# Optimization experiments

Measured on AMD Instinct MI355X. Metric: run time of the kernel, lower is better.

The kernel has to match this reference:

```python
import jax, jax.numpy as jnp
import numpy as np

DIM = 512
N_EMBED = 4096
B, T = 16, 4096


def setup_inputs() -> dict:
    key = jax.random.key(0)
    kx, ke = jax.random.split(key)
    x = jax.random.normal(kx, (B, T, DIM), dtype=jnp.float32)
    embed = jax.random.normal(ke, (DIM, N_EMBED), dtype=jnp.float32)  # codebook buffer
    return {"x": x, "embed": embed}


def reference(x, embed):
    dim = x.shape[-1]
    flatten = x.reshape(-1, dim)  # [N, dim]
    # squared L2 distance to each codebook vector: ||f||^2 - 2 f.e + ||e||^2
    dist = (
        jnp.sum(flatten * flatten, axis=1, keepdims=True)
        - 2.0 * (flatten @ embed)
        + jnp.sum(embed * embed, axis=0, keepdims=True)
    )  # [N, n_embed]
    embed_ind = jnp.argmin(dist, axis=1).reshape(x.shape[:-1])  # [B, T]
    quantize = jnp.take(embed.T, embed_ind, axis=0)  # [B, T, dim]
    diff = jnp.mean((jax.lax.stop_gradient(quantize) - x) ** 2)
    # straight-through estimator
    quantize_st = x + jax.lax.stop_gradient(quantize - x)
    return quantize_st, diff, embed_ind
```

## Files before the change

### kernel.cpp

```cpp
#include <hip/hip_runtime.h>
#include <math.h>

#define DIM 512
#define NE 4096
#define NROWS 65536
#define MARGIN 0.6f

typedef __attribute__((ext_vector_type(8))) short short8;
typedef __attribute__((ext_vector_type(4))) float f32x4;

__device__ inline unsigned short f2bf(float f) {
    union { float f; unsigned int u; } v; v.f = f;
    unsigned int u = v.u;
    return (unsigned short)((u + 0x7fffu + ((u >> 16) & 1u)) >> 16);
}
__device__ inline float bf2f(unsigned short h) {
    union { unsigned int u; float f; } v; v.u = ((unsigned int)h) << 16;
    return v.f;
}
__device__ inline short hi_bf(float f) { return (short)f2bf(f); }

__device__ inline bool lexlt(float v1, int i1, float v2, int i2) {
    return (v1 < v2) || (v1 == v2 && i1 < i2);
}

__device__ __forceinline__ size_t ehf_idx(int e, int d) {
    return (size_t)(e >> 5) * 16384 +
           (size_t)(((((d >> 5) * 2 + ((e >> 4) & 1)) * 64) + ((d >> 3) & 3) * 16 + (e & 15)) * 8 + (d & 7));
}

typedef __attribute__((address_space(1))) const void gconst_t;
typedef __attribute__((address_space(3))) void ldsv_t;
__device__ __forceinline__ void gload_lds16(const void* g, void* l) {
    __builtin_amdgcn_global_load_lds((gconst_t*)g, (ldsv_t*)l, 16, 0, 0);
}

__global__ void norms_kernel(const float* __restrict__ embed, float* __restrict__ norms) {
    int e = blockIdx.x * blockDim.x + threadIdx.x;
    if (e < NE) {
        float s = 0.f;
        #pragma unroll 8
        for (int d = 0; d < DIM; ++d) {
            float v = embed[(size_t)d * NE + e];
            s += v * v;
        }
        norms[e] = s;
    }
}

__global__ void prep_kernel(const float* __restrict__ embed,
                            unsigned short* __restrict__ ehf,
                            unsigned short* __restrict__ el) {
    __shared__ float t[64][65];
    const int tid = threadIdx.x;
    const int e0 = blockIdx.x * 64;
    const int d0 = blockIdx.y * 64;
    for (int i = tid; i < 4096; i += 256) {
        int r = i >> 6, c = i & 63;
        t[r][c] = embed[(size_t)(d0 + r) * NE + e0 + c];
    }
    __syncthreads();
    for (int i = tid; i < 4096; i += 256) {
        int r = i >> 6, c = i & 63;
        float v = t[c][r];
        int e = e0 + r, d = d0 + c;
        unsigned short h = f2bf(v);
        ehf[ehf_idx(e, d)] = h;
        el[(size_t)e * 512 + d] = f2bf(v - bf2f(h));
    }
}

__global__ __launch_bounds__(256, 2) void vq_main(
        const float* __restrict__ x,
        const unsigned short* __restrict__ ehf,
        const unsigned short* __restrict__ el,
        const float* __restrict__ norms,
        float* __restrict__ out_idx,
        int* __restrict__ idx_ws) {

    __shared__ unsigned short ph[2][32 * 512];
    __shared__ int   bi4[128][4];
    __shared__ float bgap[128];

    const int tid = threadIdx.x;
    const int w   = tid >> 6;
    const int l   = tid & 63;
    const int lr  = l & 15;
    const int lg  = l >> 4;
    const int row0 = blockIdx.x * 128;

    short8 a[2][16];
    #pragma unroll
    for (int s = 0; s < 2; ++s) {
        const float* xp = x + (size_t)(row0 + w * 32 + s * 16 + lr) * DIM + lg * 8;
        #pragma unroll
        for (int ks = 0; ks < 16; ++ks) {
            float4 u  = *(const float4*)(xp + ks * 32);
            float4 v2 = *(const float4*)(xp + ks * 32 + 4);
            short8 h;
            h[0]=hi_bf(u.x);  h[1]=hi_bf(u.y);  h[2]=hi_bf(u.z);  h[3]=hi_bf(u.w);
            h[4]=hi_bf(v2.x); h[5]=hi_bf(v2.y); h[6]=hi_bf(v2.z); h[7]=hi_bf(v2.w);
            a[s][ks] = h;
        }
    }

    float t1v[2][4], t2v[2][4]; int t1i[2][4], t2i[2][4];
    #pragma unroll
    for (int s = 0; s < 2; ++s)
        #pragma unroll
        for (int r = 0; r < 4; ++r) {
            t1v[s][r]=INFINITY; t2v[s][r]=INFINITY;
            t1i[s][r]=0x7ffffffe; t2i[s][r]=0x7fffffff;
        }

    #define STAGE_PANEL(p, b)                                                   \
    {                                                                           \
        const unsigned short* gsrc = ehf + (size_t)(p) * 16384 + w * 4096 + l * 8; \
        unsigned short* ldst = &ph[b][w * 4096];                                \
        _Pragma("unroll")                                                       \
        for (int j = 0; j < 8; ++j)                                             \
            gload_lds16(gsrc + j * 512, ldst + j * 512);                        \
    }

    STAGE_PANEL(0, 0)
    __syncthreads();

    #pragma unroll 1
    for (int ct = 0; ct < 128; ++ct) {
        const int cur = ct & 1;

        if (ct < 127) STAGE_PANEL(ct + 1, cur ^ 1)

        f32x4 acc[2][2];
        #pragma unroll
        for (int s = 0; s < 2; ++s)
            #pragma unroll
            for (int cb = 0; cb < 2; ++cb) acc[s][cb] = (f32x4){0.f,0.f,0.f,0.f};

        #pragma unroll
        for (int ks = 0; ks < 16; ++ks) {
            #pragma unroll
            for (int cb = 0; cb < 2; ++cb) {
                short8 bh = *(const short8*)&ph[cur][(ks * 2 + cb) * 512 + l * 8];
                acc[0][cb] = __builtin_amdgcn_mfma_f32_16x16x32_bf16(a[0][ks], bh, acc[0][cb], 0, 0, 0);
                acc[1][cb] = __builtin_amdgcn_mfma_f32_16x16x32_bf16(a[1][ks], bh, acc[1][cb], 0, 0, 0);
            }
        }

        #pragma unroll
        for (int cb = 0; cb < 2; ++cb) {
            int e = ct * 32 + cb * 16 + lr;
            float nrm = norms[e];
            #pragma unroll
            for (int s = 0; s < 2; ++s)
                #pragma unroll
                for (int r = 0; r < 4; ++r) {
                    float sv = fmaf(-2.0f, acc[s][cb][r], nrm);
                    if (sv < t1v[s][r]) { t2v[s][r]=t1v[s][r]; t2i[s][r]=t1i[s][r]; t1v[s][r]=sv; t1i[s][r]=e; }
                    else if (sv < t2v[s][r]) { t2v[s][r]=sv; t2i[s][r]=e; }
                }
        }
        __syncthreads();
    }
    #undef STAGE_PANEL

    #pragma unroll
    for (int s = 0; s < 2; ++s) {
        #pragma unroll
        for (int r = 0; r < 4; ++r) {
            float av[4] = { t1v[s][r], t2v[s][r], INFINITY, INFINITY };
            int   ai[4] = { t1i[s][r], t2i[s][r], 0x7ffffffe, 0x7fffffff };
            #pragma unroll
            for (int m = 1; m < 16; m <<= 1) {
                float bv[4]; int bi_[4];
                #pragma unroll
                for (int q = 0; q < 4; ++q) {
                    bv[q]  = __shfl_xor(av[q], m, 64);
                    bi_[q] = __shfl_xor(ai[q], m, 64);
                }
                float cv[4]; int ci[4];
                #pragma unroll
                for (int q = 0; q < 4; ++q) {
                    bool t = lexlt(av[q], ai[q], bv[3 - q], bi_[3 - q]);
                    cv[q] = t ? av[q] : bv[3 - q];
                    ci[q] = t ? ai[q] : bi_[3 - q];
                }
                #define CE(A,B) { if (!lexlt(cv[A],ci[A],cv[B],ci[B])) { \
                    float tv=cv[A]; cv[A]=cv[B]; cv[B]=tv; int ti=ci[A]; ci[A]=ci[B]; ci[B]=ti; } }
                CE(0,2) CE(1,3) CE(0,1) CE(2,3)
                #undef CE
                #pragma unroll
                for (int q = 0; q < 4; ++q) { av[q] = cv[q]; ai[q] = ci[q]; }
            }
            if (lr == 0) {
                int rowloc = w * 32 + s * 16 + lg * 4 + r;
                #pragma unroll
                for (int q = 0; q < 4; ++q) bi4[rowloc][q] = ai[q];
                bgap[rowloc] = av[1] - av[0];
            }
        }
    }
    __syncthreads();

    #pragma unroll 1
    for (int rr = 0; rr < 32; ++rr) {
        int rowloc = w * 32 + rr;
        int grow = row0 + rowloc;
        float gap = bgap[rowloc];
        int c0 = bi4[rowloc][0] & (NE - 1);
        if (gap > MARGIN) {
            if (l == 0) { out_idx[grow] = (float)c0; idx_ws[grow] = c0; }
            continue;
        }
        int cand[4];
        cand[0] = c0;
        cand[1] = bi4[rowloc][1] & (NE - 1);
        cand[2] = bi4[rowloc][2] & (NE - 1);
        cand[3] = bi4[rowloc][3] & (NE - 1);

        const float* xr = x + (size_t)grow * DIM + l * 8;
        float4 xa = *(const float4*)xr, xb = *(const float4*)(xr + 4);
        float xv[8] = {xa.x, xa.y, xa.z, xa.w, xb.x, xb.y, xb.z, xb.w};

        float d[4];
        #pragma unroll
        for (int q = 0; q < 4; ++q) {
            uint4 hv = *(const uint4*)&ehf[ehf_idx(cand[q], l * 8)];
            uint4 lv = *(const uint4*)&el[(size_t)cand[q] * 512 + l * 8];
            const unsigned short* hp = (const unsigned short*)&hv;
            const unsigned short* lp = (const unsigned short*)&lv;
            float acc = 0.f;
            #pragma unroll
            for (int j = 0; j < 8; ++j) acc += xv[j] * (bf2f(hp[j]) + bf2f(lp[j]));
            d[q] = acc;
        }
        #pragma unroll
        for (int m = 32; m >= 1; m >>= 1) {
            #pragma unroll
            for (int q = 0; q < 4; ++q) d[q] += __shfl_xor(d[q], m, 64);
        }
        if (l == 0) {
            float bs = norms[cand[0]] - 2.0f * d[0];
            int   bi = cand[0];
            #pragma unroll
            for (int q = 1; q < 4; ++q) {
                float sq = norms[cand[q]] - 2.0f * d[q];
                if (sq < bs || (sq == bs && cand[q] < bi)) { bs = sq; bi = cand[q]; }
            }
            out_idx[grow] = (float)bi;
            idx_ws[grow] = bi;
        }
    }
}

__global__ void gather_kernel(const float* __restrict__ x,
                              const unsigned short* __restrict__ ehf,
                              const unsigned short* __restrict__ el,
                              const int* __restrict__ idx, float* __restrict__ out_q,
                              float* __restrict__ partial) {
    __shared__ float red[256];
    const int tid = threadIdx.x;
    float local = 0.f;
    #pragma unroll 1
    for (int j = 0; j < 8; ++j) {
        int o8 = blockIdx.x * 2048 + j * 256 + tid;
        int r  = o8 >> 6;
        int c8 = o8 & 63;
        int e  = idx[r];
        uint4 hv = *(const uint4*)&ehf[ehf_idx(e, c8 * 8)];
        uint4 lv = *(const uint4*)&el[(size_t)e * 512 + c8 * 8];
        const unsigned short* hp = (const unsigned short*)&hv;
        const unsigned short* lp = (const unsigned short*)&lv;
        float q[8];
        #pragma unroll
        for (int k = 0; k < 8; ++k) q[k] = bf2f(hp[k]) + bf2f(lp[k]);
        float4 xa = *(const float4*)&x[(size_t)r * DIM + c8 * 8];
        float4 xb = *(const float4*)&x[(size_t)r * DIM + c8 * 8 + 4];
        *(float4*)&out_q[(size_t)r * DIM + c8 * 8]     = make_float4(q[0], q[1], q[2], q[3]);
        *(float4*)&out_q[(size_t)r * DIM + c8 * 8 + 4] = make_float4(q[4], q[5], q[6], q[7]);
        float xs[8] = {xa.x, xa.y, xa.z, xa.w, xb.x, xb.y, xb.z, xb.w};
        #pragma unroll
        for (int k = 0; k < 8; ++k) { float t = q[k] - xs[k]; local += t * t; }
    }
    red[tid] = local;
    __syncthreads();
    for (int s = 128; s > 0; s >>= 1) {
        if (tid < s) red[tid] += red[tid + s];
        __syncthreads();
    }
    if (tid == 0) partial[blockIdx.x] = red[0];
}

__global__ void diff_kernel(const float* __restrict__ partial, float* __restrict__ out_diff) {
    __shared__ float red[256];
    float s = 0.f;
    for (int i = threadIdx.x; i < 2048; i += 256) s += partial[i];
    red[threadIdx.x] = s;
    __syncthreads();
    for (int st = 128; st > 0; st >>= 1) {
        if (threadIdx.x < st) red[threadIdx.x] += red[threadIdx.x + st];
        __syncthreads();
    }
    if (threadIdx.x == 0)
        out_diff[0] = red[0] * (1.0f / ((float)NROWS * (float)DIM));
}

#define BM 32
#define BN 64
#define BK 16
__global__ __launch_bounds__(256) void vq_kernel_fb(
        const float* __restrict__ x, const float* __restrict__ embed,
        const float* __restrict__ norms, float* __restrict__ out_q,
        float* __restrict__ out_idx, float* __restrict__ partial) {
    __shared__ float xs[BM][BK + 1];
    __shared__ float es[BK][BN];
    __shared__ float rv[BM][17];
    __shared__ int   ri[BM][17];
    __shared__ float bestv[BM];
    __shared__ int   besti[BM];
    __shared__ float red[256];
    const int tid = threadIdx.x;
    const int tc  = tid & 15;
    const int tr  = tid >> 4;
    const int row0 = blockIdx.x * BM;
    if (tid < BM) { bestv[tid] = INFINITY; besti[tid] = 0; }
    __syncthreads();
    for (int ct = 0; ct < NE / BN; ++ct) {
        float acc[2][4] = {{0.f,0.f,0.f,0.f},{0.f,0.f,0.f,0.f}};
        for (int k0 = 0; k0 < DIM; k0 += BK) {
            {
                int r = tid >> 3;
                int k = (tid & 7) * 2;
                const float* src = &x[(size_t)(row0 + r) * DIM + k0 + k];
                xs[r][k] = src[0]; xs[r][k + 1] = src[1];
            }
            {
                int r = tid >> 4;
                int c = (tid & 15) * 4;
                float4 v = *(const float4*)&embed[(size_t)(k0 + r) * NE + ct * BN + c];
                *(float4*)&es[r][c] = v;
            }
            __syncthreads();
            #pragma unroll
            for (int kk = 0; kk < BK; ++kk) {
                float a0 = xs[tr * 2 + 0][kk];
                float a1 = xs[tr * 2 + 1][kk];
                float4 b = *(const float4*)&es[kk][tc * 4];
                acc[0][0] += a0 * b.x; acc[0][1] += a0 * b.y;
                acc[0][2] += a0 * b.z; acc[0][3] += a0 * b.w;
                acc[1][0] += a1 * b.x; acc[1][1] += a1 * b.y;
                acc[1][2] += a1 * b.z; acc[1][3] += a1 * b.w;
            }
            __syncthreads();
        }
        #pragma unroll
        for (int i = 0; i < 2; ++i) {
            float bv = INFINITY; int bj = 0;
            #pragma unroll
            for (int j = 0; j < 4; ++j) {
                int e = ct * BN + tc * 4 + j;
                float s = norms[e] - 2.0f * acc[i][j];
                if (s < bv) { bv = s; bj = e; }
            }
            rv[tr * 2 + i][tc] = bv; ri[tr * 2 + i][tc] = bj;
        }
        __syncthreads();
        if (tid < BM) {
            float bv = bestv[tid]; int bi = besti[tid];
            #pragma unroll
            for (int t = 0; t < 16; ++t) {
                float v = rv[tid][t];
                if (v < bv) { bv = v; bi = ri[tid][t]; }
            }
            bestv[tid] = bv; besti[tid] = bi;
        }
        __syncthreads();
    }
    if (tid < BM) out_idx[row0 + tid] = (float)besti[tid];
    __syncthreads();
    float local = 0.f;
    for (int i = tid; i < BM * DIM; i += 256) {
        int r = i >> 9;
        int d = i & (DIM - 1);
        int e = besti[r];
        float q  = embed[(size_t)d * NE + e];
        float xv = x[(size_t)(row0 + r) * DIM + d];
        out_q[(size_t)(row0 + r) * DIM + d] = q;
        float t = q - xv;
        local += t * t;
    }
    red[tid] = local;
    __syncthreads();
    for (int s = 128; s > 0; s >>= 1) {
        if (tid < s) red[tid] += red[tid + s];
        __syncthreads();
    }
    if (tid == 0) partial[blockIdx.x] = red[0];
}

extern "C" void kernel_launch(void* const* d_in, const int* in_sizes, int n_in,
                              void* d_out, int out_size, void* d_ws, size_t ws_size,
                              hipStream_t stream) {
    (void)in_sizes; (void)n_in; (void)out_size;
    const float* x     = (const float*)d_in[0];
    const float* embed = (const float*)d_in[1];

    float* out      = (float*)d_out;
    float* out_q    = out;
    float* out_diff = out + (size_t)NROWS * DIM;
    float* out_idx  = out_diff + 1;

    const size_t NEED = 4194304ull * 2 + 16384 + 8192 + 262144;

    char* wsb = (char*)d_ws;
    if (ws_size >= NEED) {
        unsigned short* ehf     = (unsigned short*)wsb;
        unsigned short* el      = (unsigned short*)(wsb + 4194304);
        float*          norms   = (float*)(wsb + 8388608);
        float*          partial = (float*)(wsb + 8404992);
        int*            idx     = (int*)(wsb + 8413184);

        norms_kernel<<<NE / 256, 256, 0, stream>>>(embed, norms);
        prep_kernel<<<dim3(64, 8), 256, 0, stream>>>(embed, ehf, el);
        vq_main<<<512, 256, 0, stream>>>(x, ehf, el, norms, out_idx, idx);
        gather_kernel<<<2048, 256, 0, stream>>>(x, ehf, el, idx, out_q, partial);
        diff_kernel<<<1, 256, 0, stream>>>(partial, out_diff);
    } else {
        float* norms   = (float*)wsb;
        float* partial = norms + NE;
        norms_kernel<<<NE / 256, 256, 0, stream>>>(embed, norms);
        vq_kernel_fb<<<NROWS / BM, 256, 0, stream>>>(x, embed, norms, out_q, out_idx, partial);
        diff_kernel<<<1, 256, 0, stream>>>(partial, out_diff);
    }
}
```

Before: 469.9 us.

## Software-pipeline MFMA with epilogue and pack distance and index into one key

The codebook panel loop now keeps two sets of accumulators. The MFMAs for panel i+1 are issued while the top-2 epilogue for panel i runs, so matrix math overlaps the scalar compare work. The top-2 tracking and the cross-lane merge replace branchy float/index comparisons with branchless unsigned min/max on a single key: the float distance bits with the low 12 mantissa bits replaced by the codebook index. That key truncation costs distance precision, so the rescoring margin is raised from 0.6 to 1.0, which may send more rows to the exact fallback. Ordering raw float bits as unsigned integers is only correct for non-negative distances.

Result: faster. 416.2 us (-11.4%).

```diff
diff --git a/kernel.cpp b/kernel.cpp
--- a/kernel.cpp
+++ b/kernel.cpp
@@ -4,7 +4,7 @@
 #define DIM 512
 #define NE 4096
 #define NROWS 65536
-#define MARGIN 0.6f
+#define MARGIN 1.0f
 
 typedef __attribute__((ext_vector_type(8))) short short8;
 typedef __attribute__((ext_vector_type(4))) float f32x4;
@@ -19,10 +19,6 @@
     return v.f;
 }
 __device__ inline short hi_bf(float f) { return (short)f2bf(f); }
-
-__device__ inline bool lexlt(float v1, int i1, float v2, int i2) {
-    return (v1 < v2) || (v1 == v2 && i1 < i2);
-}
 
 __device__ __forceinline__ size_t ehf_idx(int e, int d) {
     return (size_t)(e >> 5) * 16384 +
@@ -104,99 +100,111 @@
         }
     }
 
-    float t1v[2][4], t2v[2][4]; int t1i[2][4], t2i[2][4];
+    unsigned p1[2][4], p2[2][4];
     #pragma unroll
     for (int s = 0; s < 2; ++s)
         #pragma unroll
-        for (int r = 0; r < 4; ++r) {
-            t1v[s][r]=INFINITY; t2v[s][r]=INFINITY;
-            t1i[s][r]=0x7ffffffe; t2i[s][r]=0x7fffffff;
-        }
-
-    #define STAGE_PANEL(p, b)                                                   \
-    {                                                                           \
+        for (int r = 0; r < 4; ++r) { p1[s][r] = 0xFFFFFFFFu; p2[s][r] = 0xFFFFFFFFu; }
+
+    f32x4 accA[2][2], accB[2][2];
+
+    #define STAGE_PANEL(p, b)                                                      \
+    {                                                                              \
         const unsigned short* gsrc = ehf + (size_t)(p) * 16384 + w * 4096 + l * 8; \
-        unsigned short* ldst = &ph[b][w * 4096];                                \
-        _Pragma("unroll")                                                       \
-        for (int j = 0; j < 8; ++j)                                             \
-            gload_lds16(gsrc + j * 512, ldst + j * 512);                        \
+        unsigned short* ldst = &ph[b][w * 4096];                                   \
+        _Pragma("unroll")                                                          \
+        for (int j = 0; j < 8; ++j)                                                \
+            gload_lds16(gsrc + j * 512, ldst + j * 512);                           \
+    }
+
+    #define MFMA_PANEL(ACC, BUF)                                                   \
+    {                                                                              \
+        _Pragma("unroll")                                                          \
+        for (int s = 0; s < 2; ++s)                                                \
+            _Pragma("unroll")                                                      \
+            for (int cb = 0; cb < 2; ++cb) ACC[s][cb] = (f32x4){0.f,0.f,0.f,0.f};  \
+        _Pragma("unroll")                                                          \
+        for (int ks = 0; ks < 16; ++ks) {                                          \
+            _Pragma("unroll")                                                      \
+            for (int cb = 0; cb < 2; ++cb) {                                       \
+                short8 bh = *(const short8*)&ph[BUF][(ks * 2 + cb) * 512 + l * 8]; \
+                ACC[0][cb] = __builtin_amdgcn_mfma_f32_16x16x32_bf16(a[0][ks], bh, ACC[0][cb], 0, 0, 0); \
+                ACC[1][cb] = __builtin_amdgcn_mfma_f32_16x16x32_bf16(a[1][ks], bh, ACC[1][cb], 0, 0, 0); \
+            }                                                                      \
+        }                                                                          \
+    }
+
+    #define EPIL_PANEL(ACC, PANEL)                                                 \
+    {                                                                              \
+        _Pragma("unroll")                                                          \
+        for (int cb = 0; cb < 2; ++cb) {                                           \
+            int e = (PANEL) * 32 + cb * 16 + lr;                                   \
+            float nrm = norms[e];                                                  \
+            _Pragma("unroll")                                                      \
+            for (int s = 0; s < 2; ++s)                                            \
+                _Pragma("unroll")                                                  \
+                for (int r = 0; r < 4; ++r) {                                      \
+                    float sv = fmaf(-2.0f, ACC[s][cb][r], nrm);                    \
+                    unsigned pv = (__float_as_uint(sv) & 0xFFFFF000u) | (unsigned)e; \
+                    unsigned t = max(p1[s][r], pv);                                \
+                    p1[s][r] = min(p1[s][r], pv);                                  \
+                    p2[s][r] = min(p2[s][r], t);                                   \
+                }                                                                  \
+        }                                                                          \
     }
 
     STAGE_PANEL(0, 0)
     __syncthreads();
+    STAGE_PANEL(1, 1)
+    MFMA_PANEL(accA, 0)
+    __syncthreads();
 
     #pragma unroll 1
-    for (int ct = 0; ct < 128; ++ct) {
-        const int cur = ct & 1;
-
-        if (ct < 127) STAGE_PANEL(ct + 1, cur ^ 1)
-
-        f32x4 acc[2][2];
-        #pragma unroll
-        for (int s = 0; s < 2; ++s)
-            #pragma unroll
-            for (int cb = 0; cb < 2; ++cb) acc[s][cb] = (f32x4){0.f,0.f,0.f,0.f};
-
-        #pragma unroll
-        for (int ks = 0; ks < 16; ++ks) {
-            #pragma unroll
-            for (int cb = 0; cb < 2; ++cb) {
-                short8 bh = *(const short8*)&ph[cur][(ks * 2 + cb) * 512 + l * 8];
-                acc[0][cb] = __builtin_amdgcn_mfma_f32_16x16x32_bf16(a[0][ks], bh, acc[0][cb], 0, 0, 0);
-                acc[1][cb] = __builtin_amdgcn_mfma_f32_16x16x32_bf16(a[1][ks], bh, acc[1][cb], 0, 0, 0);
-            }
-        }
-
-        #pragma unroll
-        for (int cb = 0; cb < 2; ++cb) {
-            int e = ct * 32 + cb * 16 + lr;
-            float nrm = norms[e];
-            #pragma unroll
-            for (int s = 0; s < 2; ++s)
-                #pragma unroll
-                for (int r = 0; r < 4; ++r) {
-                    float sv = fmaf(-2.0f, acc[s][cb][r], nrm);
-                    if (sv < t1v[s][r]) { t2v[s][r]=t1v[s][r]; t2i[s][r]=t1i[s][r]; t1v[s][r]=sv; t1i[s][r]=e; }
-                    else if (sv < t2v[s][r]) { t2v[s][r]=sv; t2i[s][r]=e; }
-                }
-        }
-        __syncthreads();
-    }
+    for (int i = 1; i < 127; i += 2) {
+        STAGE_PANEL(i + 1, 0)
+        MFMA_PANEL(accB, 1)
+        EPIL_PANEL(accA, i - 1)
+        __syncthreads();
+        if (i + 2 < 128) STAGE_PANEL(i + 2, 1)
+        MFMA_PANEL(accA, 0)
+        EPIL_PANEL(accB, i)
+        __syncthreads();
+    }
+    MFMA_PANEL(accB, 1)
+    EPIL_PANEL(accA, 126)
+    EPIL_PANEL(accB, 127)
+
     #undef STAGE_PANEL
+    #undef MFMA_PANEL
+    #undef EPIL_PANEL
 
     #pragma unroll
     for (int s = 0; s < 2; ++s) {
         #pragma unroll
         for (int r = 0; r < 4; ++r) {
-            float av[4] = { t1v[s][r], t2v[s][r], INFINITY, INFINITY };
-            int   ai[4] = { t1i[s][r], t2i[s][r], 0x7ffffffe, 0x7fffffff };
+            unsigned av[4] = { p1[s][r], p2[s][r], 0xFFFFFFFFu, 0xFFFFFFFFu };
             #pragma unroll
             for (int m = 1; m < 16; m <<= 1) {
-                float bv[4]; int bi_[4];
+                unsigned bv[4];
                 #pragma unroll
-                for (int q = 0; q < 4; ++q) {
-                    bv[q]  = __shfl_xor(av[q], m, 64);
-                    bi_[q] = __shfl_xor(ai[q], m, 64);
-                }
-                float cv[4]; int ci[4];
+                for (int q = 0; q < 4; ++q)
+                    bv[q] = (unsigned)__shfl_xor((int)av[q], m, 64);
+                unsigned cv[4];
                 #pragma unroll
-                for (int q = 0; q < 4; ++q) {
-                    bool t = lexlt(av[q], ai[q], bv[3 - q], bi_[3 - q]);
-                    cv[q] = t ? av[q] : bv[3 - q];
-                    ci[q] = t ? ai[q] : bi_[3 - q];
-                }
-                #define CE(A,B) { if (!lexlt(cv[A],ci[A],cv[B],ci[B])) { \
-                    float tv=cv[A]; cv[A]=cv[B]; cv[B]=tv; int ti=ci[A]; ci[A]=ci[B]; ci[B]=ti; } }
+                for (int q = 0; q < 4; ++q) cv[q] = min(av[q], bv[3 - q]);
+                #define CE(A,B) { unsigned lo = min(cv[A], cv[B]); unsigned hi = max(cv[A], cv[B]); cv[A] = lo; cv[B] = hi; }
                 CE(0,2) CE(1,3) CE(0,1) CE(2,3)
                 #undef CE
                 #pragma unroll
-                for (int q = 0; q < 4; ++q) { av[q] = cv[q]; ai[q] = ci[q]; }
+                for (int q = 0; q < 4; ++q) av[q] = cv[q];
             }
             if (lr == 0) {
                 int rowloc = w * 32 + s * 16 + lg * 4 + r;
                 #pragma unroll
-                for (int q = 0; q < 4; ++q) bi4[rowloc][q] = ai[q];
-                bgap[rowloc] = av[1] - av[0];
+                for (int q = 0; q < 4; ++q) bi4[rowloc][q] = (int)av[q];
+                float v0 = __uint_as_float(av[0] & 0xFFFFF000u);
+                float v1 = __uint_as_float(av[1] & 0xFFFFF000u);
+                bgap[rowloc] = v1 - v0;
             }
         }
     }
```
